# Optimization experiments

Measured on AMD Instinct MI355X. Metric: run time of the kernel, lower is better.

Reference implementation:

```python
import jax, jax.numpy as jnp
import numpy as np

B, N, F, H, A, T = 4, 256, 64, 256, 16, 3


def setup_inputs() -> dict:
    key = jax.random.key(0)
    ks = jax.random.split(key, 18)
    s = 0.05
    rn = lambda k, shp: jax.random.normal(k, shp, dtype=jnp.float32) * s
    return {
        "node_features": jax.random.normal(ks[0], (B, N, F), dtype=jnp.float32),
        "adjacency": jax.random.randint(ks[1], (B, N, N), 0, 2).astype(jnp.int32),
        # preprocess MLP: F->H->H
        "pre_W1": rn(ks[2], (F, H)), "pre_b1": jnp.zeros((H,), jnp.float32),
        "pre_W2": rn(ks[3], (H, H)), "pre_b2": jnp.zeros((H,), jnp.float32),
        # message MLP: 2H->H->H
        "msg_W1": rn(ks[4], (2 * H, H)), "msg_b1": jnp.zeros((H,), jnp.float32),
        "msg_W2": rn(ks[5], (H, H)), "msg_b2": jnp.zeros((H,), jnp.float32),
        # GRUCell params (jax layout [in, 3H]; gate order r,z,n like torch)
        "gru_Wih": rn(ks[6], (H, 3 * H)), "gru_Whh": rn(ks[7], (H, 3 * H)),
        "gru_bih": jnp.zeros((3 * H,), jnp.float32), "gru_bhh": jnp.zeros((3 * H,), jnp.float32),
        # readout MLP: H->H->A
        "ro_W1": rn(ks[8], (H, H)), "ro_b1": jnp.zeros((H,), jnp.float32),
        "ro_W2": rn(ks[9], (H, A)), "ro_b2": jnp.zeros((A,), jnp.float32),
    }


def reference(node_features, adjacency, pre_W1, pre_b1, pre_W2, pre_b2,
              msg_W1, msg_b1, msg_W2, msg_b2,
              gru_Wih, gru_Whh, gru_bih, gru_bhh,
              ro_W1, ro_b1, ro_W2, ro_b2):
    adj = adjacency.astype(node_features.dtype)  # [B,N,N]
    # preprocess: Linear-ReLU-Linear
    h = jnp.maximum(node_features @ pre_W1 + pre_b1, 0.0) @ pre_W2 + pre_b2  # [B,N,H]

    W1_i, W1_j = msg_W1[:H], msg_W1[H:]  # concat([h_i,h_j]) @ W1 == h_i@W1_i + h_j@W1_j
    for _ in range(T):
        hi = h @ W1_i  # [B,N,H] receiver part
        hj = h @ W1_j  # [B,N,H] sender part
        e = jnp.maximum(hi[:, :, None, :] + hj[:, None, :, :] + msg_b1, 0.0)  # [B,N,N,H]
        m = e @ msg_W2 + msg_b2  # [B,N,N,H] messages
        agg = jnp.einsum('bijh,bij->bih', m, adj)  # mask + sum over senders j
        # GRUCell(input=agg, hidden=h), torch gate order (r, z, n)
        gi = agg @ gru_Wih + gru_bih  # [B,N,3H]
        gh = h @ gru_Whh + gru_bhh
        ir, iz, inn = jnp.split(gi, 3, axis=-1)
        hr, hz, hn = jnp.split(gh, 3, axis=-1)
        r = jax.nn.sigmoid(ir + hr)
        z = jax.nn.sigmoid(iz + hz)
        n = jnp.tanh(inn + r * hn)
        h = (1.0 - z) * n + z * h

    g = jnp.sum(h, axis=1)  # [B,H] graph readout
    q = jnp.maximum(g @ ro_W1 + ro_b1, 0.0) @ ro_W2 + ro_b2  # [B,A]
    return q
```

## Files before the change

kernel.cpp:

```cpp
#include <hip/hip_runtime.h>
#include <hip/hip_bf16.h>


typedef unsigned short ushort_t;
typedef short bf8_t __attribute__((ext_vector_type(8)));
typedef float f4_t  __attribute__((ext_vector_type(4)));

#define BN_ROWS 1024

#define UB_NFB    0
#define UB_PW1T   65536
#define UB_PW2T   81920
#define UB_WCATT  147456
#define UB_WGT    475136
#define UB_H2     917504
#define UB_EHAT2  1441792

#define F_PREB1   1015808
#define F_PREB2   1016064
#define F_BCAT    1016320
#define F_BIH     1017600
#define F_ROW1    1018368
#define F_ROB1    1083904
#define F_ROW2    1084160
#define F_ROB2    1088256
#define F_H       1088272
#define F_HCAT    1350416
#define F_FLAG    2661136
#define F_GCNT    2661140

#define CVa 65536
#define CVb 81920
#define CVc 147456
#define CVd 475136
#define CV_TOTAL 547600
#define NCONV 1070

__device__ __forceinline__ float bf2f(ushort_t u) {
    return __uint_as_float(((unsigned int)u) << 16);
}
__device__ __forceinline__ ushort_t f2b(float v) {
    __hip_bfloat16 b = __float2bfloat16(v);
    return *reinterpret_cast<ushort_t*>(&b);
}
__device__ __forceinline__ float relu(float v) { return v < 0.f ? 0.f : v; }
__device__ __forceinline__ float ld(const void* p, int i, int isf32) {
    return isf32 ? ((const float*)p)[i] : bf2f(((const ushort_t*)p)[i]);
}

__global__ __launch_bounds__(256) void convwg_kernel(
    const void* nf, const void* preW1, const void* preb1, const void* preW2, const void* preb2,
    const void* msgW1, const void* msgb1, const void* msgW2, const void* msgb2,
    const void* gruWih, const void* gruWhh, const void* grubih, const void* grubhh,
    const void* roW1, const void* rob1, const void* roW2, const void* rob2,
    float* __restrict__ w)
{
    __shared__ float w2s[4 * 256];
    __shared__ int cnt;
    const int t = threadIdx.x;
    ushort_t* wb = (ushort_t*)w;

    if (t == 0) cnt = 0;
    __syncthreads();
    {
        const ushort_t* nf0 = (const ushort_t*)nf;
        int bad = 0;
        for (int i = 0; i < 8; ++i) {
            ushort_t u = nf0[(t * 8 + i) * 2];
            int ex = (u >> 7) & 0xFF;
            if ((u & 0x7fff) != 0 && (ex < 100 || ex > 140)) bad++;
        }
        atomicAdd(&cnt, bad);
    }
    __syncthreads();
    const int f32 = (cnt > 512) ? 1 : 0;

    if (blockIdx.x == 0) {
        if (t < 4) ((int*)(w + F_GCNT))[t] = 0;
        if (t == 4) *(int*)(w + F_FLAG) = f32;
    }

    if (blockIdx.x < NCONV) {
        const int e0 = (blockIdx.x * 256 + t) * 2;
#pragma unroll
        for (int u2 = 0; u2 < 2; ++u2) {
            int e = e0 + u2;
            if (e >= CV_TOTAL) break;
            if (e < CVa) {
                wb[UB_NFB + e] = f2b(ld(nf, e, f32));
            } else if (e < CVb) {
                int i = e - CVa; int n = i >> 6, k = i & 63;
                wb[UB_PW1T + i] = f2b(ld(preW1, k * 256 + n, f32));
            } else if (e < CVc) {
                int i = e - CVb; int n = i >> 8, k = i & 255;
                wb[UB_PW2T + i] = f2b(ld(preW2, k * 256 + n, f32));
            } else if (e < CVd) {
                int i = e - CVc; int n = i >> 8, k = i & 255;
                float v;
                if (n < 256)      v = ld(msgW1, k * 256 + n, f32);
                else if (n < 512) v = ld(msgW1, (256 + k) * 256 + (n - 256), f32);
                else              v = ld(gruWhh, k * 768 + (n - 512), f32);
                wb[UB_WCATT + i] = f2b(v);
            } else {
                int f = e - CVd;
                float v;
                if (f < 256)        v = ld(preb1, f, f32);
                else if (f < 512)   v = ld(preb2, f - 256, f32);
                else if (f < 1792) {
                    int c = f - 512;
                    if (c < 256)      v = ld(msgb1, c, f32);
                    else if (c < 512) v = 0.f;
                    else              v = ld(grubhh, c - 512, f32);
                }
                else if (f < 2560)  v = ld(grubih, f - 1792, f32);
                else if (f < 68096) v = ld(roW1, f - 2560, f32);
                else if (f < 68352) v = ld(rob1, f - 68096, f32);
                else if (f < 72448) v = ld(roW2, f - 68352, f32);
                else                v = ld(rob2, f - 72448, f32);
                w[F_PREB1 + f] = v;
            }
        }
        return;
    }

    const int wt = blockIdx.x - NCONV;
    const int p0 = (wt % 3) * 256;
    const int k0 = (wt / 3) * 4;
    for (int i = t; i < 4 * 256; i += 256) {
        int r = i >> 8, n = i & 255;
        int krow = k0 + r;
        float v;
        if (krow < 256)       v = ld(msgW2, krow * 256 + n, f32);
        else if (krow == 256) v = ld(msgb2, n, f32);
        else                  v = 0.f;
        w2s[i] = v;
    }
    __syncthreads();
    const int p = p0 + t;
    float acc4[4] = {};
    for (int n0 = 0; n0 < 256; n0 += 32) {
        float wv[32];
#pragma unroll
        for (int i = 0; i < 32; ++i)
            wv[i] = ld(gruWih, (n0 + i) * 768 + p, f32);
#pragma unroll
        for (int r = 0; r < 4; ++r) {
            float acc = acc4[r];
#pragma unroll
            for (int q = 0; q < 8; ++q) {
                f4_t w4 = *(const f4_t*)&w2s[r * 256 + n0 + q * 4];
                acc += w4[0] * wv[q * 4 + 0] + w4[1] * wv[q * 4 + 1]
                     + w4[2] * wv[q * 4 + 2] + w4[3] * wv[q * 4 + 3];
            }
            acc4[r] = acc;
        }
    }
#pragma unroll
    for (int r = 0; r < 4; ++r) {
        int krow = k0 + r;
        ushort_t hi = f2b(acc4[r]);
        ushort_t lo = f2b(acc4[r] - bf2f(hi));
        wb[UB_WGT + p * 576 + krow] = hi;
        wb[UB_WGT + p * 576 + 288 + krow] = lo;
    }
}

__global__ __launch_bounds__(256) void prenet_kernel(float* __restrict__ w)
{
    __shared__ ushort_t As[32 * 64];
    __shared__ ushort_t Xs[32 * 256];
    __shared__ ushort_t Bs[256 * 32];
    ushort_t* wb = (ushort_t*)w;
    const int t = threadIdx.x;
    const int wave = t >> 6, lane = t & 63;
    const int ln = lane & 15, quad = lane >> 4;
    const int wr = (wave & 1) * 16, wc = (wave >> 1) * 128;
    const int rbase = blockIdx.x * 32;
    const int srow = t >> 2, skc = (t & 3) << 3;

    {
        int row = t >> 3, kc = (t & 7) << 3;
        *(bf8_t*)(&As[row * 64 + kc]) =
            *(const bf8_t*)(&wb[UB_NFB + (rbase + row) * 64 + kc]);
    }

    f4_t acc[8] = {};
    for (int k0 = 0; k0 < 64; k0 += 32) {
        __syncthreads();
#pragma unroll
        for (int rr = 0; rr < 4; ++rr) {
            int n = srow + 64 * rr;
            *(bf8_t*)(&Bs[n * 32 + skc]) =
                *(const bf8_t*)(&wb[UB_PW1T + n * 64 + k0 + skc]);
        }
        __syncthreads();
        bf8_t af = *(const bf8_t*)(&As[(wr + ln) * 64 + k0 + quad * 8]);
#pragma unroll
        for (int n = 0; n < 8; ++n) {
            bf8_t bfr = *(const bf8_t*)(&Bs[(wc + n * 16 + ln) * 32 + quad * 8]);
            acc[n] = __builtin_amdgcn_mfma_f32_16x16x32_bf16(af, bfr, acc[n], 0, 0, 0);
        }
    }
    __syncthreads();
#pragma unroll
    for (int n = 0; n < 8; ++n) {
        int col = wc + n * 16 + ln;
        float bb = w[F_PREB1 + col];
#pragma unroll
        for (int r = 0; r < 4; ++r) {
            int row = wr + quad * 4 + r;
            Xs[row * 256 + col] = f2b(relu(acc[n][r] + bb));
        }
        acc[n] = (f4_t){0.f, 0.f, 0.f, 0.f};
    }
    __syncthreads();

    for (int k0 = 0; k0 < 256; k0 += 32) {
        __syncthreads();
#pragma unroll
        for (int rr = 0; rr < 4; ++rr) {
            int n = srow + 64 * rr;
            *(bf8_t*)(&Bs[n * 32 + skc]) =
                *(const bf8_t*)(&wb[UB_PW2T + n * 256 + k0 + skc]);
        }
        __syncthreads();
        bf8_t af = *(const bf8_t*)(&Xs[(wr + ln) * 256 + k0 + quad * 8]);
#pragma unroll
        for (int n = 0; n < 8; ++n) {
            bf8_t bfr = *(const bf8_t*)(&Bs[(wc + n * 16 + ln) * 32 + quad * 8]);
            acc[n] = __builtin_amdgcn_mfma_f32_16x16x32_bf16(af, bfr, acc[n], 0, 0, 0);
        }
    }
#pragma unroll
    for (int n = 0; n < 8; ++n) {
        int col = wc + n * 16 + ln;
        float bb = w[F_PREB2 + col];
#pragma unroll
        for (int r = 0; r < 4; ++r) {
            int grow = rbase + wr + quad * 4 + r;
            float v = acc[n][r] + bb;
            w[F_H + grow * 256 + col] = v;
            ushort_t hi = f2b(v);
            wb[UB_H2 + grow * 512 + col] = hi;
            wb[UB_H2 + grow * 512 + 256 + col] = f2b(v - bf2f(hi));
        }
    }
}

#define HLD 104
__global__ __launch_bounds__(256) void hcat_kernel(float* __restrict__ w)
{
    __shared__ ushort_t As[32 * HLD];
    __shared__ ushort_t Bs[128 * HLD];
    ushort_t* wb = (ushort_t*)w;
    const ushort_t* A  = wb + UB_H2;
    const ushort_t* Bt = wb + UB_WCATT;
    const int t = threadIdx.x;
    const int wave = t >> 6, lane = t & 63;
    const int ln = lane & 15, quad = lane >> 4;
    const int bm = (blockIdx.x & 31) * 32, bn = (blockIdx.x >> 5) * 128;
    const int wm = (wave >> 1) * 16, wn = (wave & 1) * 64;

    const int arow = t >> 3, akc = (t & 7) << 3;
    const int agoff = (bm + arow) * 512 + akc;
    const int aloff = arow * HLD + akc;
    int bgoff[4], bloff[4];
#pragma unroll
    for (int i = 0; i < 4; ++i) {
        int slot = i * 256 + t;
        int brow = slot >> 3, bkc = (slot & 7) << 3;
        bgoff[i] = (bn + brow) * 256 + bkc;
        bloff[i] = brow * HLD + bkc;
    }

    f4_t acc[4] = {};
    bf8_t ra, rb[4];

    ra = *(const bf8_t*)(&A[agoff]);
#pragma unroll
    for (int i = 0; i < 4; ++i)
        rb[i] = *(const bf8_t*)(&Bt[bgoff[i]]);

    for (int ks = 0; ks < 8; ++ks) {
        __syncthreads();
        *(bf8_t*)(&As[aloff]) = ra;
#pragma unroll
        for (int i = 0; i < 4; ++i)
            *(bf8_t*)(&Bs[bloff[i]]) = rb[i];
        __syncthreads();
        if (ks < 7) {
            int k0 = (ks + 1) * 64;
            int kb = k0 & 255;
            ra = *(const bf8_t*)(&A[agoff + k0]);
#pragma unroll
            for (int i = 0; i < 4; ++i)
                rb[i] = *(const bf8_t*)(&Bt[bgoff[i] + kb]);
        }
#pragma unroll
        for (int kk = 0; kk < 2; ++kk) {
            bf8_t af = *(const bf8_t*)(&As[(wm + ln) * HLD + kk * 32 + quad * 8]);
#pragma unroll
            for (int ni = 0; ni < 4; ++ni) {
                bf8_t bfr = *(const bf8_t*)(&Bs[(wn + ni * 16 + ln) * HLD + kk * 32 + quad * 8]);
                acc[ni] = __builtin_amdgcn_mfma_f32_16x16x32_bf16(af, bfr, acc[ni], 0, 0, 0);
            }
        }
    }

#pragma unroll
    for (int ni = 0; ni < 4; ++ni) {
        int col = bn + wn + ni * 16 + ln;
        float bb = w[F_BCAT + col];
#pragma unroll
        for (int r = 0; r < 4; ++r) {
            int row = bm + wm + quad * 4 + r;
            w[F_HCAT + row * 1280 + col] = acc[ni][r] + bb;
        }
    }
}

__global__ __launch_bounds__(256) void msg_kernel(
    const float* __restrict__ hcat,
    const int*   __restrict__ adj,
    ushort_t* __restrict__ ehat)
{
    const int row = blockIdx.x;
    const int t = threadIdx.x;
    __shared__ int ej[256];
    __shared__ int ecnt;
    if (t == 0) ecnt = 0;
    __syncthreads();
    if (adj[row * 256 + t]) { int p = atomicAdd(&ecnt, 1); ej[p] = t; }
    const float hi = hcat[row * 1280 + t];
    const float* hjb = hcat + (row >> 8) * 256 * 1280 + 256;
    __syncthreads();
    const int ne = ecnt;
    float acc = 0.f;
#pragma unroll 4
    for (int p = 0; p < ne; ++p) {
        int j = ej[p];
        acc += relu(hi + hjb[j * 1280 + t]);
    }
    ushort_t h16 = f2b(acc);
    ushort_t l16 = f2b(acc - bf2f(h16));
    ushort_t* er = ehat + row * 576;
    er[t] = h16;
    er[288 + t] = l16;
    if (t < 32) {
        er[256 + t] = f2b(t == 0 ? (float)ne : 0.f);
        er[544 + t] = 0;
    }
}

#define GLD 104
template<int FINAL>
__global__ __launch_bounds__(256) void gigru_kernel(float* __restrict__ w,
                                                    void* __restrict__ out)
{
    __shared__ ushort_t As[16 * GLD];
    __shared__ ushort_t Bs[192 * GLD];
    __shared__ float gl[256];
    __shared__ float t1[256];
    __shared__ int donef;
    ushort_t* wb = (ushort_t*)w;
    const int t = threadIdx.x;
    const int wave = t >> 6, lane = t & 63;
    const int ln = lane & 15, quad = lane >> 4;
    const int xcd = blockIdx.x & 7;
    const int cg = xcd & 3;
    const int rg = (blockIdx.x >> 3) + 32 * (xcd >> 2);
    const int rbase = rg * 16;

    const int aval = (t < 192);
    const int arow = t / 12, akc = (t % 12) * 8;
    const int agoff = (rbase + arow) * 576 + akc;
    const int aloff = arow * GLD + akc;
    int bgoff[9], bloff[9];
#pragma unroll
    for (int i = 0; i < 9; ++i) {
        int slot = i * 256 + t;
        int brow = slot / 12, bkc = (slot % 12) * 8;
        int wrow = (brow >> 6) * 256 + cg * 64 + (brow & 63);
        bgoff[i] = wrow * 576 + bkc;
        bloff[i] = brow * GLD + bkc;
    }
    const ushort_t* Ehp = wb + UB_EHAT2;
    const ushort_t* Bp  = wb + UB_WGT;

    f4_t acc[3] = {};
    bf8_t ra, rb[9];

    if (aval) ra = *(const bf8_t*)(&Ehp[agoff]);
#pragma unroll
    for (int i = 0; i < 9; ++i)
        rb[i] = *(const bf8_t*)(&Bp[bgoff[i]]);

    for (int ks = 0; ks < 9; ++ks) {
        __syncthreads();
        if (aval) *(bf8_t*)(&As[aloff]) = ra;
#pragma unroll
        for (int i = 0; i < 9; ++i)
            *(bf8_t*)(&Bs[bloff[i]]) = rb[i];
        __syncthreads();
        if (ks < 8) {
            int k0 = (ks + 1) * 96;
            int ka = (k0 < 576) ? k0 : k0 - 576;
            int kb = (k0 < 288) ? k0 : k0 - 288;
            if (aval) ra = *(const bf8_t*)(&Ehp[agoff + ka]);
#pragma unroll
            for (int i = 0; i < 9; ++i)
                rb[i] = *(const bf8_t*)(&Bp[bgoff[i] + kb]);
        }
#pragma unroll
        for (int kk = 0; kk < 3; ++kk) {
            bf8_t af = *(const bf8_t*)(&As[ln * GLD + kk * 32 + quad * 8]);
#pragma unroll
            for (int n = 0; n < 3; ++n) {
                int fn = wave + n * 4;
                bf8_t bfr = *(const bf8_t*)(&Bs[(fn * 16 + ln) * GLD + kk * 32 + quad * 8]);
                acc[n] = __builtin_amdgcn_mfma_f32_16x16x32_bf16(af, bfr, acc[n], 0, 0, 0);
            }
        }
    }

    {
        const int col = cg * 64 + wave * 16 + ln;
        float bi_r = w[F_BIH + col];
        float bi_z = w[F_BIH + 256 + col];
        float bi_n = w[F_BIH + 512 + col];
#pragma unroll
        for (int r = 0; r < 4; ++r) {
            int row = rbase + quad * 4 + r;
            float ir = acc[0][r] + bi_r;
            float iz = acc[1][r] + bi_z;
            float in = acc[2][r] + bi_n;
            const float* ghr = w + F_HCAT + row * 1280 + 512;
            float hr = ghr[col], hz = ghr[256 + col], hn = ghr[512 + col];
            float rg_ = 1.f / (1.f + __expf(-(ir + hr)));
            float z   = 1.f / (1.f + __expf(-(iz + hz)));
            float nn  = tanhf(in + rg_ * hn);
            float ho = w[F_H + row * 256 + col];
            float hv = (1.f - z) * nn + z * ho;
            w[F_H + row * 256 + col] = hv;
            if (!FINAL) {
                ushort_t hb = f2b(hv);
                wb[UB_H2 + row * 512 + col] = hb;
                wb[UB_H2 + row * 512 + 256 + col] = f2b(hv - bf2f(hb));
            }
        }
    }

    if (FINAL) {
        const int g = rg >> 4;
        __syncthreads();
        if (t == 0) {
            __threadfence();
            int prev = atomicAdd((int*)(w + F_GCNT) + g, 1);
            donef = (prev == 63);
        }
        __syncthreads();
        if (!donef) return;
        __threadfence();

        const float* hb = w + F_H + g * 256 * 256;
        float s = 0.f;
        for (int n = 0; n < 256; ++n) s += hb[n * 256 + t];
        gl[t] = s;
        __syncthreads();
        float acc1 = w[F_ROB1 + t];
        for (int k = 0; k < 256; ++k) acc1 += gl[k] * w[F_ROW1 + k * 256 + t];
        t1[t] = relu(acc1);
        __syncthreads();
        if (t < 16) {
            float q = w[F_ROB2 + t];
            for (int k = 0; k < 256; ++k) q += t1[k] * w[F_ROW2 + k * 16 + t];
            if (*(const int*)(w + F_FLAG)) ((float*)out)[g * 16 + t] = q;
            else ((__hip_bfloat16*)out)[g * 16 + t] = __float2bfloat16(q);
        }
    }
}

extern "C" void kernel_launch(void* const* d_in, const int* in_sizes, int n_in,
                              void* d_out, int out_size, void* d_ws, size_t ws_size,
                              hipStream_t stream) {
    float* w = (float*)d_ws;
    ushort_t* wb = (ushort_t*)d_ws;

    static const int dictSz[18]  = {65536,262144,16384,256,65536,256,131072,256,65536,256,
                                    196608,196608,768,768,65536,256,4096,16};
    static const int alphaSz[18] = {262144,196608,196608,768,768,131072,65536,256,256,
                                    65536,16384,65536,256,256,65536,4096,256,16};
    static const int alphaPos[18] = {9,0,10,12,11,13,5,7,6,8,2,1,4,3,14,16,15,17};
    bool dictOK = true, alphaOK = true;
    for (int i = 0; i < 18 && i < n_in; ++i) {
        if (in_sizes[i] != dictSz[i])  dictOK = false;
        if (in_sizes[i] != alphaSz[i]) alphaOK = false;
    }
    const void* P[18];
    for (int l = 0; l < 18; ++l) P[l] = d_in[(!dictOK && alphaOK) ? alphaPos[l] : l];
    const int* adj = (const int*)P[1];

    convwg_kernel<<<NCONV + 216, 256, 0, stream>>>(
        P[0], P[2], P[3], P[4], P[5], P[6], P[7], P[8], P[9],
        P[10], P[11], P[12], P[13], P[14], P[15], P[16], P[17], w);

    prenet_kernel<<<32, 256, 0, stream>>>(w);

    for (int it = 0; it < 3; ++it) {
        hcat_kernel<<<320, 256, 0, stream>>>(w);
        msg_kernel<<<BN_ROWS, 256, 0, stream>>>(w + F_HCAT, adj, wb + UB_EHAT2);
        if (it < 2)
            gigru_kernel<0><<<256, 256, 0, stream>>>(w, d_out);
        else
            gigru_kernel<1><<<256, 256, 0, stream>>>(w, d_out);
    }
}
```

Measured before the change: 265.3 us.

## Move h@Whh GEMM from hcat kernel into gigru kernel epilogue

The hidden-state GRU projection (h@Whh) is no longer computed by the hcat kernel and written to global memory. The gigru kernel now runs a second bf16 MFMA GEMM over the split-bf16 hidden state and consumes the result directly in registers. hcat shrinks to 512 columns and launches 128 blocks instead of 320, which cuts global stores and reloads of the 768-wide gh buffer. In exchange, gigru does more work per block with an extra K loop, and gh precision now depends on split-bf16 MFMA rather than the earlier path.

```diff
diff --git a/kernel.cpp b/kernel.cpp
--- a/kernel.cpp
+++ b/kernel.cpp
@@ -314,7 +314,7 @@
 #pragma unroll
         for (int r = 0; r < 4; ++r) {
             int row = bm + wm + quad * 4 + r;
-            w[F_HCAT + row * 1280 + col] = acc[ni][r] + bb;
+            w[F_HCAT + row * 512 + col] = acc[ni][r] + bb;
         }
     }
 }
@@ -331,15 +331,15 @@
     if (t == 0) ecnt = 0;
     __syncthreads();
     if (adj[row * 256 + t]) { int p = atomicAdd(&ecnt, 1); ej[p] = t; }
-    const float hi = hcat[row * 1280 + t];
-    const float* hjb = hcat + (row >> 8) * 256 * 1280 + 256;
+    const float hi = hcat[row * 512 + t];
+    const float* hjb = hcat + (row >> 8) * 256 * 512 + 256;
     __syncthreads();
     const int ne = ecnt;
     float acc = 0.f;
 #pragma unroll 4
     for (int p = 0; p < ne; ++p) {
         int j = ej[p];
-        acc += relu(hi + hjb[j * 1280 + t]);
+        acc += relu(hi + hjb[j * 512 + t]);
     }
     ushort_t h16 = f2b(acc);
     ushort_t l16 = f2b(acc - bf2f(h16));
@@ -388,37 +388,90 @@
     const ushort_t* Bp  = wb + UB_WGT;
 
     f4_t acc[3] = {};
-    bf8_t ra, rb[9];
-
-    if (aval) ra = *(const bf8_t*)(&Ehp[agoff]);
-#pragma unroll
-    for (int i = 0; i < 9; ++i)
-        rb[i] = *(const bf8_t*)(&Bp[bgoff[i]]);
-
-    for (int ks = 0; ks < 9; ++ks) {
-        __syncthreads();
-        if (aval) *(bf8_t*)(&As[aloff]) = ra;
+    {
+        bf8_t ra, rb[9];
+        if (aval) ra = *(const bf8_t*)(&Ehp[agoff]);
 #pragma unroll
         for (int i = 0; i < 9; ++i)
-            *(bf8_t*)(&Bs[bloff[i]]) = rb[i];
-        __syncthreads();
-        if (ks < 8) {
-            int k0 = (ks + 1) * 96;
-            int ka = (k0 < 576) ? k0 : k0 - 576;
-            int kb = (k0 < 288) ? k0 : k0 - 288;
-            if (aval) ra = *(const bf8_t*)(&Ehp[agoff + ka]);
+            rb[i] = *(const bf8_t*)(&Bp[bgoff[i]]);
+
+        for (int ks = 0; ks < 9; ++ks) {
+            __syncthreads();
+            if (aval) *(bf8_t*)(&As[aloff]) = ra;
 #pragma unroll
             for (int i = 0; i < 9; ++i)
-                rb[i] = *(const bf8_t*)(&Bp[bgoff[i] + kb]);
-        }
-#pragma unroll
-        for (int kk = 0; kk < 3; ++kk) {
-            bf8_t af = *(const bf8_t*)(&As[ln * GLD + kk * 32 + quad * 8]);
-#pragma unroll
-            for (int n = 0; n < 3; ++n) {
-                int fn = wave + n * 4;
-                bf8_t bfr = *(const bf8_t*)(&Bs[(fn * 16 + ln) * GLD + kk * 32 + quad * 8]);
-                acc[n] = __builtin_amdgcn_mfma_f32_16x16x32_bf16(af, bfr, acc[n], 0, 0, 0);
+                *(bf8_t*)(&Bs[bloff[i]]) = rb[i];
+            __syncthreads();
+            if (ks < 8) {
+                int k0 = (ks + 1) * 96;
+                int ka = (k0 < 576) ? k0 : k0 - 576;
+                int kb = (k0 < 288) ? k0 : k0 - 288;
+                if (aval) ra = *(const bf8_t*)(&Ehp[agoff + ka]);
+#pragma unroll
+                for (int i = 0; i < 9; ++i)
+                    rb[i] = *(const bf8_t*)(&Bp[bgoff[i] + kb]);
+            }
+#pragma unroll
+            for (int kk = 0; kk < 3; ++kk) {
+                bf8_t af = *(const bf8_t*)(&As[ln * GLD + kk * 32 + quad * 8]);
+#pragma unroll
+                for (int n = 0; n < 3; ++n) {
+                    int fn = wave + n * 4;
+                    bf8_t bfr = *(const bf8_t*)(&Bs[(fn * 16 + ln) * GLD + kk * 32 + quad * 8]);
+                    acc[n] = __builtin_amdgcn_mfma_f32_16x16x32_bf16(af, bfr, acc[n], 0, 0, 0);
+                }
+            }
+        }
+    }
+
+    const int aval2 = (t < 128);
+    const int arow2 = t >> 3, akc2 = (t & 7) << 3;
+    const int agoff2 = (rbase + arow2) * 512 + akc2;
+    const int aloff2 = arow2 * GLD + akc2;
+    int bgoff2[6], bloff2[6];
+#pragma unroll
+    for (int i = 0; i < 6; ++i) {
+        int slot = i * 256 + t;
+        int brow = slot >> 3, bkc = (slot & 7) << 3;
+        int wrow = 512 + (brow >> 6) * 256 + cg * 64 + (brow & 63);
+        bgoff2[i] = wrow * 256 + bkc;
+        bloff2[i] = brow * GLD + bkc;
+    }
+    const ushort_t* Hp = wb + UB_H2;
+    const ushort_t* Wp = wb + UB_WCATT;
+
+    f4_t acch[3] = {};
+    {
+        bf8_t ra, rb[6];
+        if (aval2) ra = *(const bf8_t*)(&Hp[agoff2]);
+#pragma unroll
+        for (int i = 0; i < 6; ++i)
+            rb[i] = *(const bf8_t*)(&Wp[bgoff2[i]]);
+
+        for (int ks = 0; ks < 8; ++ks) {
+            __syncthreads();
+            if (aval2) *(bf8_t*)(&As[aloff2]) = ra;
+#pragma unroll
+            for (int i = 0; i < 6; ++i)
+                *(bf8_t*)(&Bs[bloff2[i]]) = rb[i];
+            __syncthreads();
+            if (ks < 7) {
+                int k0 = (ks + 1) * 64;
+                int kb = k0 & 255;
+                if (aval2) ra = *(const bf8_t*)(&Hp[agoff2 + k0]);
+#pragma unroll
+                for (int i = 0; i < 6; ++i)
+                    rb[i] = *(const bf8_t*)(&Wp[bgoff2[i] + kb]);
+            }
+#pragma unroll
+            for (int kk = 0; kk < 2; ++kk) {
+                bf8_t af = *(const bf8_t*)(&As[ln * GLD + kk * 32 + quad * 8]);
+#pragma unroll
+                for (int n = 0; n < 3; ++n) {
+                    int fn = wave + n * 4;
+                    bf8_t bfr = *(const bf8_t*)(&Bs[(fn * 16 + ln) * GLD + kk * 32 + quad * 8]);
+                    acch[n] = __builtin_amdgcn_mfma_f32_16x16x32_bf16(af, bfr, acch[n], 0, 0, 0);
+                }
             }
         }
     }
@@ -428,14 +481,18 @@
         float bi_r = w[F_BIH + col];
         float bi_z = w[F_BIH + 256 + col];
         float bi_n = w[F_BIH + 512 + col];
+        float bh_r = w[F_BCAT + 512 + col];
+        float bh_z = w[F_BCAT + 768 + col];
+        float bh_n = w[F_BCAT + 1024 + col];
 #pragma unroll
         for (int r = 0; r < 4; ++r) {
             int row = rbase + quad * 4 + r;
             float ir = acc[0][r] + bi_r;
             float iz = acc[1][r] + bi_z;
             float in = acc[2][r] + bi_n;
-            const float* ghr = w + F_HCAT + row * 1280 + 512;
-            float hr = ghr[col], hz = ghr[256 + col], hn = ghr[512 + col];
+            float hr = acch[0][r] + bh_r;
+            float hz = acch[1][r] + bh_z;
+            float hn = acch[2][r] + bh_n;
             float rg_ = 1.f / (1.f + __expf(-(ir + hr)));
             float z   = 1.f / (1.f + __expf(-(iz + hz)));
             float nn  = tanhf(in + rg_ * hn);
@@ -507,7 +564,7 @@
     prenet_kernel<<<32, 256, 0, stream>>>(w);
 
     for (int it = 0; it < 3; ++it) {
-        hcat_kernel<<<320, 256, 0, stream>>>(w);
+        hcat_kernel<<<128, 256, 0, stream>>>(w);
         msg_kernel<<<BN_ROWS, 256, 0, stream>>>(w + F_HCAT, adj, wb + UB_EHAT2);
         if (it < 2)
             gigru_kernel<0><<<256, 256, 0, stream>>>(w, d_out);
```

After: 262.7 us. Within noise of the previous version (-1.0%).
